# Kernel optimization log

Measured on AMD Instinct MI355X. Metric: run time of the kernel, lower is better.

Reference implementation:

```python
import jax, jax.numpy as jnp
import numpy as np

N_NODES = 50000
N_EDGES = 800000
D_IN, D_HID, N_CLS, N_PROT = 128, 256, 16, 512
EPS = 1e-6


def setup_inputs() -> dict:
    key = jax.random.key(0)
    ks = jax.random.split(key, 12)
    s = 0.05
    return {
        "x": jax.random.normal(ks[0], (N_NODES, D_IN), dtype=jnp.float32),
        "edge_index": jax.random.randint(ks[1], (2, N_EDGES), 0, N_NODES, dtype=jnp.int64),
        "prot": jax.random.randint(ks[2], (N_PROT,), 0, N_NODES, dtype=jnp.int64),
        "epoch": 1,
        "W0": jax.random.normal(ks[3], (D_IN, D_HID), dtype=jnp.float32) * s,
        "b0": jnp.zeros((D_HID,), jnp.float32),
        "W1": jax.random.normal(ks[4], (D_HID, D_HID), dtype=jnp.float32) * s,
        "b1": jnp.zeros((D_HID,), jnp.float32),
        "Wl1": jax.random.normal(ks[5], (D_HID, D_HID), dtype=jnp.float32) * s,
        "bl1": jnp.zeros((D_HID,), jnp.float32),
        "Wl2": jax.random.normal(ks[6], (D_HID, N_CLS), dtype=jnp.float32) * s,
        "bl2": jnp.zeros((N_CLS,), jnp.float32),
    }


def _gcn_layer(h, W, b, src, dst, norm, n):
    # PyG GCNConv: h' = scatter_add(norm * (h @ W)[src] -> dst) + b
    m = (h @ W)[src] * norm[:, None]
    return jax.ops.segment_sum(m, dst, num_segments=n) + b


def _forward(x, edge_index, prot, W0, b0, W1, b1, Wl1, bl1, Wl2, bl2):
    n = x.shape[0]
    loops = jnp.arange(n, dtype=edge_index.dtype)
    src = jnp.concatenate([edge_index[0], loops])
    dst = jnp.concatenate([edge_index[1], loops])
    deg = jax.ops.segment_sum(jnp.ones_like(dst, dtype=x.dtype), dst, num_segments=n)
    dis = jax.lax.rsqrt(deg)  # deg >= 1 thanks to self loops
    norm = dis[src] * dis[dst]

    h = jax.nn.relu(_gcn_layer(x, W0, b0, src, dst, norm, n))
    h = _gcn_layer(h, W1, b1, src, dst, norm, n)

    # L2 row-normalize (torch divides by the norm directly)
    qn = jnp.linalg.norm(h, axis=1, keepdims=True)
    h = h / qn

    # relative_rep: cosine similarity of every node to each anchor
    anchors = h[prot]                             # [P, H]
    nx = jnp.linalg.norm(h, axis=1)               # [N]
    na = jnp.linalg.norm(anchors, axis=1)         # [P]
    num = h @ anchors.T                           # [N, P]
    x_rel = num / jnp.maximum(nx[:, None] * na[None, :], EPS)

    # classifier head on prototypes -> out_proto, then composed prediction
    lin = lambda z: jax.nn.relu(z @ Wl1 + bl1) @ Wl2 + bl2
    out_proto = jax.nn.log_softmax(lin(anchors), axis=-1)   # [P, C]
    out = jax.nn.log_softmax(x_rel @ out_proto, axis=-1)    # [N, C]
    return out, x_rel, out_proto


def reference(x, edge_index, prot, epoch, W0, b0, W1, b1, Wl1, bl1, Wl2, bl2):
    # epoch >= first_step_epochs (=0) branch: inference-path composition
    return _forward(x, edge_index, prot, W0, b0, W1, b1, Wl1, bl1, Wl2, bl2)


if __name__ == "__main__":
    out, x_rel, out_proto = reference(**setup_inputs())
    print(out.shape, x_rel.shape, out_proto.shape)
```

## Files before the change

### kernel.cpp

```cpp
#include <hip/hip_runtime.h>
#include <hip/hip_bf16.h>
#include <math.h>

#define NN 50000
#define NP 50048
#define EE 800000
#define EPAD 1150016
#define DIN 128
#define HID 256
#define NCLS 16
#define NPROT 512

typedef __attribute__((ext_vector_type(8))) short short8;
typedef __attribute__((ext_vector_type(4))) float f32x4;
typedef unsigned int u32;
typedef unsigned long long u64;

__device__ inline unsigned short f2b(float f) {
    union { float f; unsigned u; } c; c.f = f;
    unsigned u = c.u;
    unsigned r = (u + 0x7FFFu + ((u >> 16) & 1u)) >> 16;
    return (unsigned short)r;
}
__device__ inline float b2f(unsigned short u) {
    union { unsigned u; float f; } c; c.u = ((unsigned)u) << 16; return c.f;
}

#define GL2LDS16(g, l)                                                              \
    __builtin_amdgcn_global_load_lds(                                               \
        (const __attribute__((address_space(1))) unsigned int*)(g),                 \
        (__attribute__((address_space(3))) unsigned int*)(l), 16, 0, 0)


__global__ __launch_bounds__(256) void k_count(const int* __restrict__ dst, int* __restrict__ cnt, int e) {
    int i = blockIdx.x * 256 + threadIdx.x;
    if (i < e) atomicAdd(&cnt[dst[i]], 1);
}

__global__ __launch_bounds__(256) void k_scan1(const int* __restrict__ cnt, int* __restrict__ excl,
                                               int* __restrict__ bsum, float* __restrict__ dis, int n) {
    __shared__ int s[256];
    int t = threadIdx.x;
    int i = blockIdx.x * 256 + t;
    int v = (i < n) ? cnt[i] : 0;
    if (i < n) dis[i] = rsqrtf((float)v + 1.0f);
    int vp = (v + 7) & ~7;
    s[t] = vp; __syncthreads();
    for (int d = 1; d < 256; d <<= 1) {
        int add = (t >= d) ? s[t - d] : 0;
        __syncthreads();
        s[t] += add;
        __syncthreads();
    }
    if (i < n) excl[i] = s[t] - vp;
    if (t == 255) bsum[blockIdx.x] = s[255];
}

__global__ __launch_bounds__(256) void k_scan2(const int* __restrict__ bsum, int* __restrict__ boff, int nb) {
    __shared__ int s[256];
    int t = threadIdx.x;
    int v = (t < nb) ? bsum[t] : 0;
    s[t] = v; __syncthreads();
    for (int d = 1; d < 256; d <<= 1) {
        int add = (t >= d) ? s[t - d] : 0;
        __syncthreads();
        s[t] += add;
        __syncthreads();
    }
    if (t < nb) boff[t] = s[t] - v;
}

__global__ __launch_bounds__(256) void k_scan3(const int* __restrict__ excl, const int* __restrict__ boff,
                                               const int* __restrict__ bsum,
                                               int* __restrict__ off, int n, int nb) {
    int i = blockIdx.x * 256 + threadIdx.x;
    if (i < n) off[i] = excl[i] + boff[blockIdx.x];
    if (i == 0) off[n] = boff[nb - 1] + bsum[nb - 1];
}

__global__ __launch_bounds__(256) void k_fill(const int* __restrict__ src, const int* __restrict__ dst,
                                              const int* __restrict__ off, int* __restrict__ cursor,
                                              const float* __restrict__ dis,
                                              int2* __restrict__ csr_e, int e) {
    int i = blockIdx.x * 256 + threadIdx.x;
    if (i >= e) return;
    int s = src[i], d = dst[i];
    int pos = atomicAdd(&cursor[d], 1);
    csr_e[off[d] + pos] = make_int2(s, __float_as_int(dis[s] * dis[d]));
}


#define CAST_BLKS (NN * DIN / 4 / 256)
#define WT0_BLKS  (DIN * HID / 256)
#define WT1_BLKS  (HID * HID / 256)

__global__ __launch_bounds__(256) void k_prep(const float* __restrict__ x, unsigned short* __restrict__ xb,
                                              const float* __restrict__ W0, unsigned short* __restrict__ Wt0,
                                              const float* __restrict__ W1, unsigned short* __restrict__ Wt1) {
    int b = blockIdx.x, t = threadIdx.x;
    if (b < CAST_BLKS) {
        int i = b * 256 + t;
        float4 v = ((const float4*)x)[i];
        ushort4 o; o.x = f2b(v.x); o.y = f2b(v.y); o.z = f2b(v.z); o.w = f2b(v.w);
        ((ushort4*)xb)[i] = o;
    } else if (b < CAST_BLKS + WT0_BLKS) {
        int i = (b - CAST_BLKS) * 256 + t;
        int k = i / HID, n = i - k * HID;
        Wt0[n * DIN + k] = f2b(W0[(size_t)k * HID + n]);
    } else {
        int i = (b - CAST_BLKS - WT0_BLKS) * 256 + t;
        int k = i / HID, n = i - k * HID;
        Wt1[n * HID + k] = f2b(W1[(size_t)k * HID + n]);
    }
}


__global__ __launch_bounds__(256) void k_gemm_mfma(const unsigned short* __restrict__ A,
                                                   const unsigned short* __restrict__ Bt,
                                                   void* __restrict__ C, int M, int Nc, int K, int mode,
                                                   const float* __restrict__ bias) {
    __shared__ __align__(16) unsigned short As[128 * 32];
    __shared__ __align__(16) unsigned short Bs[128 * 32];
    const int t = threadIdx.x;
    const int lane = t & 63;
    const int quad = lane >> 4;
    const int l16 = lane & 15;
    const int wv = t >> 6;
    const int wm = (wv & 1) * 64, wn = (wv >> 1) * 64;
    const int m0 = blockIdx.y * 128, n0 = blockIdx.x * 128;

    f32x4 acc[4][4];
#pragma unroll
    for (int i = 0; i < 4; ++i)
#pragma unroll
        for (int j = 0; j < 4; ++j)
#pragma unroll
            for (int r = 0; r < 4; ++r) acc[i][j][r] = 0.0f;

    const int sr = t >> 2;
    const int sc = (t & 3) * 8;

    for (int k0 = 0; k0 < K; k0 += 32) {
        GL2LDS16(A + (size_t)(m0 + sr) * K + k0 + sc,       &As[t * 8]);
        GL2LDS16(A + (size_t)(m0 + 64 + sr) * K + k0 + sc,  &As[2048 + t * 8]);
        GL2LDS16(Bt + (size_t)(n0 + sr) * K + k0 + sc,      &Bs[t * 8]);
        GL2LDS16(Bt + (size_t)(n0 + 64 + sr) * K + k0 + sc, &Bs[2048 + t * 8]);
        __syncthreads();
        short8 af[4], bf[4];
#pragma unroll
        for (int i = 0; i < 4; ++i)
            af[i] = *(const short8*)&As[(wm + i * 16 + l16) * 32 + quad * 8];
#pragma unroll
        for (int j = 0; j < 4; ++j)
            bf[j] = *(const short8*)&Bs[(wn + j * 16 + l16) * 32 + quad * 8];
#pragma unroll
        for (int i = 0; i < 4; ++i)
#pragma unroll
            for (int j = 0; j < 4; ++j)
                acc[i][j] = __builtin_amdgcn_mfma_f32_16x16x32_bf16(af[i], bf[j], acc[i][j], 0, 0, 0);
        __syncthreads();
    }

#pragma unroll
    for (int i = 0; i < 4; ++i) {
        int rb = m0 + wm + i * 16 + quad * 4;
#pragma unroll
        for (int j = 0; j < 4; ++j) {
            int col = n0 + wn + j * 16 + l16;
#pragma unroll
            for (int rg = 0; rg < 4; ++rg) {
                int r = rb + rg;
                float v = acc[i][j][rg];
                if (mode == 0) {
                    ((unsigned short*)C)[(size_t)r * Nc + col] = f2b(v);
                } else {
                    v = fmaxf(v + bias[col], 0.0f);
                    ((unsigned short*)C)[(size_t)r * Nc + col] = f2b(v);
                }
            }
        }
    }
}


#define GATHER8_D(go, ga)                                                      \
    asm volatile(                                                              \
        "global_load_dword %0, %[g0], off\n\t"                                 \
        "global_load_dword %1, %[g1], off\n\t"                                 \
        "global_load_dword %2, %[g2], off\n\t"                                 \
        "global_load_dword %3, %[g3], off\n\t"                                 \
        "global_load_dword %4, %[g4], off\n\t"                                 \
        "global_load_dword %5, %[g5], off\n\t"                                 \
        "global_load_dword %6, %[g6], off\n\t"                                 \
        "global_load_dword %7, %[g7], off\n\t"                                 \
        "s_waitcnt vmcnt(0)"                                                   \
        : "=&v"(go[0]), "=&v"(go[1]), "=&v"(go[2]), "=&v"(go[3]),              \
          "=&v"(go[4]), "=&v"(go[5]), "=&v"(go[6]), "=&v"(go[7])               \
        : [g0]"v"(ga[0]), [g1]"v"(ga[1]), [g2]"v"(ga[2]), [g3]"v"(ga[3]),      \
          [g4]"v"(ga[4]), [g5]"v"(ga[5]), [g6]"v"(ga[6]), [g7]"v"(ga[7])       \
        : "memory")

#define GATHER8_D2(go, ga)                                                     \
    asm volatile(                                                              \
        "global_load_dwordx2 %0, %[g0], off\n\t"                               \
        "global_load_dwordx2 %1, %[g1], off\n\t"                               \
        "global_load_dwordx2 %2, %[g2], off\n\t"                               \
        "global_load_dwordx2 %3, %[g3], off\n\t"                               \
        "global_load_dwordx2 %4, %[g4], off\n\t"                               \
        "global_load_dwordx2 %5, %[g5], off\n\t"                               \
        "global_load_dwordx2 %6, %[g6], off\n\t"                               \
        "global_load_dwordx2 %7, %[g7], off\n\t"                               \
        "s_waitcnt vmcnt(0)"                                                   \
        : "=&v"(go[0]), "=&v"(go[1]), "=&v"(go[2]), "=&v"(go[3]),              \
          "=&v"(go[4]), "=&v"(go[5]), "=&v"(go[6]), "=&v"(go[7])               \
        : [g0]"v"(ga[0]), [g1]"v"(ga[1]), [g2]"v"(ga[2]), [g3]"v"(ga[3]),      \
          [g4]"v"(ga[4]), [g5]"v"(ga[5]), [g6]"v"(ga[6]), [g7]"v"(ga[7])       \
        : "memory")

__global__ __launch_bounds__(256) void k_agg128(const unsigned short* __restrict__ xw, const int* __restrict__ off,
                                                const int2* __restrict__ csr, const float* __restrict__ dis,
                                                unsigned short* __restrict__ out, int n) {
    int node = (blockIdx.x * 256 + threadIdx.x) >> 6;
    int lane = threadIdx.x & 63;
    if (node >= n) return;
    float d = dis[node];
    float w0 = d * d;
    ushort2 u = ((const ushort2*)(xw + (size_t)node * DIN))[lane];
    float a0 = w0 * b2f(u.x), a1 = w0 * b2f(u.y);
    int p = off[node], p1 = off[node + 1];
    u64 lbase = (u64)xw + (u64)((unsigned)lane * 4u);
    while (p < p1) {
        int seg = min(p1 - p, 64);
        int2 di = csr[p + (lane < seg ? lane : 0)];
        for (int b = 0; b < seg; b += 8) {
            u64 ga[8];
            int wi[8];
#pragma unroll
            for (int k = 0; k < 8; ++k) {
                int srcn = __builtin_amdgcn_readlane(di.x, b + k);
                wi[k] = __builtin_amdgcn_readlane(di.y, b + k);
                ga[k] = lbase + (u64)((u32)srcn * (u32)(DIN * 2));
            }
            u32 go[8];
            GATHER8_D(go, ga);
#pragma unroll
            for (int k = 0; k < 8; ++k) {
                float w = __int_as_float(wi[k]);
                a0 = fmaf(w, b2f((unsigned short)go[k]), a0);
                a1 = fmaf(w, b2f((unsigned short)(go[k] >> 16)), a1);
            }
        }
        p += seg;
    }
    ushort2 o; o.x = f2b(a0); o.y = f2b(a1);
    ((ushort2*)(out + (size_t)node * DIN))[lane] = o;
}

__global__ __launch_bounds__(256) void k_agg256(const unsigned short* __restrict__ xw, const int* __restrict__ off,
                                                const int2* __restrict__ csr, const float* __restrict__ dis,
                                                const float* __restrict__ bias,
                                                unsigned short* __restrict__ out, float* __restrict__ nx, int n) {
    int node = (blockIdx.x * 256 + threadIdx.x) >> 6;
    int lane = threadIdx.x & 63;
    if (node >= n) return;
    float d = dis[node];
    float w0 = d * d;
    ushort4 u = ((const ushort4*)(xw + (size_t)node * HID))[lane];
    float a0 = w0 * b2f(u.x), a1 = w0 * b2f(u.y), a2 = w0 * b2f(u.z), a3 = w0 * b2f(u.w);
    int p = off[node], p1 = off[node + 1];
    u64 lbase = (u64)xw + (u64)((unsigned)lane * 8u);
    while (p < p1) {
        int seg = min(p1 - p, 64);
        int2 di = csr[p + (lane < seg ? lane : 0)];
        for (int b = 0; b < seg; b += 8) {
            u64 ga[8];
            int wi[8];
#pragma unroll
            for (int k = 0; k < 8; ++k) {
                int srcn = __builtin_amdgcn_readlane(di.x, b + k);
                wi[k] = __builtin_amdgcn_readlane(di.y, b + k);
                ga[k] = lbase + (u64)((u32)srcn * (u32)(HID * 2));
            }
            u64 go[8];
            GATHER8_D2(go, ga);
#pragma unroll
            for (int k = 0; k < 8; ++k) {
                float w = __int_as_float(wi[k]);
                u32 lo = (u32)go[k], hi = (u32)(go[k] >> 32);
                a0 = fmaf(w, b2f((unsigned short)lo), a0);
                a1 = fmaf(w, b2f((unsigned short)(lo >> 16)), a1);
                a2 = fmaf(w, b2f((unsigned short)hi), a2);
                a3 = fmaf(w, b2f((unsigned short)(hi >> 16)), a3);
            }
        }
        p += seg;
    }
    float4 b = ((const float4*)bias)[lane];
    a0 += b.x; a1 += b.y; a2 += b.z; a3 += b.w;
    float ss = a0 * a0 + a1 * a1 + a2 * a2 + a3 * a3;
    for (int m = 32; m >= 1; m >>= 1) ss += __shfl_xor(ss, m, 64);
    float qn = sqrtf(ss);
    a0 /= qn; a1 /= qn; a2 /= qn; a3 /= qn;
    float s2 = a0 * a0 + a1 * a1 + a2 * a2 + a3 * a3;
    for (int m = 32; m >= 1; m >>= 1) s2 += __shfl_xor(s2, m, 64);
    if (lane == 0) nx[node] = sqrtf(s2);
    ushort4 o; o.x = f2b(a0); o.y = f2b(a1); o.z = f2b(a2); o.w = f2b(a3);
    ((ushort4*)(out + (size_t)node * HID))[lane] = o;
}


__global__ __launch_bounds__(256) void k_gproto(const unsigned short* __restrict__ hb,
                                                const int* __restrict__ prot, const float* __restrict__ nx,
                                                unsigned short* __restrict__ aRb, float* __restrict__ na,
                                                const float* __restrict__ Wl1, const float* __restrict__ bl1,
                                                const float* __restrict__ Wl2, const float* __restrict__ bl2,
                                                float* __restrict__ outp) {
    __shared__ float sa[HID];
    __shared__ float st[HID];
    int row = blockIdx.x, t = threadIdx.x;
    int p = prot[row];
    unsigned short us = hb[(size_t)p * HID + t];
    aRb[(size_t)row * HID + t] = us;
    sa[t] = b2f(us);
    if (t == 0) na[row] = nx[p];
    __syncthreads();
    float acc = bl1[t];
#pragma unroll 8
    for (int k = 0; k < HID; ++k) acc = fmaf(sa[k], Wl1[k * HID + t], acc);
    st[t] = fmaxf(acc, 0.0f);
    __syncthreads();
    if (t < 64) {
        int c = t & 15, ch = t >> 4;
        float z = 0.f;
#pragma unroll 8
        for (int k = ch * 64; k < ch * 64 + 64; ++k) z = fmaf(st[k], Wl2[k * NCLS + c], z);
        z += __shfl_xor(z, 16, 64);
        z += __shfl_xor(z, 32, 64);
        z += bl2[c];
        float m = z;
        for (int d = 8; d >= 1; d >>= 1) m = fmaxf(m, __shfl_xor(m, d, 64));
        float e = expf(z - m);
        float s = e;
        for (int d = 8; d >= 1; d >>= 1) s += __shfl_xor(s, d, 64);
        if (t < 16) outp[row * NCLS + c] = z - m - logf(s);
    }
}


#define XSW(row, cs) (((cs) ^ (((row) & 7) << 3)))
#define NWGX (4 * (NP / 128))

__global__ __launch_bounds__(256, 4) void k_xrel_out(const unsigned short* __restrict__ A,
                                                     const unsigned short* __restrict__ Bt,
                                                     const float* __restrict__ nx, const float* __restrict__ na,
                                                     const float* __restrict__ proto,
                                                     float* __restrict__ xrel, float* __restrict__ opart) {
    __shared__ __align__(16) unsigned short smem_us[18560];

    const int bid = blockIdx.x;
    const int q = NWGX / 8, r = NWGX % 8;
    const int xcd = bid & 7, li = bid >> 3;
    const int wk = (xcd < r ? xcd * (q + 1) : r * (q + 1) + (xcd - r) * q) + li;
    const int m0 = (wk >> 2) * 128;
    const int nc = wk & 3;
    const int n0 = nc * 128;

    const int t = threadIdx.x;
    const int lane = t & 63;
    const int quad = lane >> 4;
    const int l16 = lane & 15;
    const int wv = t >> 6;
    const int wm = (wv & 1) * 64, wn = (wv >> 1) * 64;

    float nxv[4][4];
#pragma unroll
    for (int i = 0; i < 4; ++i)
#pragma unroll
        for (int rg = 0; rg < 4; ++rg) {
            int rr = m0 + wm + i * 16 + quad * 4 + rg;
            nxv[i][rg] = nx[rr < NN ? rr : NN - 1];
        }
    float nav[4];
#pragma unroll
    for (int j = 0; j < 4; ++j) nav[j] = na[n0 + wn + j * 16 + l16];

    const int sr = t >> 2;
    const int sc = (t & 3) * 8;

    f32x4 acc[4][4];
#pragma unroll
    for (int i = 0; i < 4; ++i)
#pragma unroll
        for (int j = 0; j < 4; ++j)
#pragma unroll
            for (int rr = 0; rr < 4; ++rr) acc[i][j][rr] = 0.0f;

    for (int k0 = 0; k0 < HID; k0 += 32) {
        GL2LDS16(A + (size_t)(m0 + sr) * HID + k0 + sc,        &smem_us[t * 8]);
        GL2LDS16(A + (size_t)(m0 + 64 + sr) * HID + k0 + sc,   &smem_us[2048 + t * 8]);
        GL2LDS16(Bt + (size_t)(n0 + sr) * HID + k0 + sc,       &smem_us[4096 + t * 8]);
        GL2LDS16(Bt + (size_t)(n0 + 64 + sr) * HID + k0 + sc,  &smem_us[4096 + 2048 + t * 8]);
        __syncthreads();
        short8 af[4], bf[4];
#pragma unroll
        for (int i = 0; i < 4; ++i)
            af[i] = *(const short8*)&smem_us[(wm + i * 16 + l16) * 32 + quad * 8];
#pragma unroll
        for (int j = 0; j < 4; ++j)
            bf[j] = *(const short8*)&smem_us[4096 + (wn + j * 16 + l16) * 32 + quad * 8];
#pragma unroll
        for (int i = 0; i < 4; ++i)
#pragma unroll
            for (int j = 0; j < 4; ++j)
                acc[i][j] = __builtin_amdgcn_mfma_f32_16x16x32_bf16(af[i], bf[j], acc[i][j], 0, 0, 0);
        __syncthreads();
    }

    for (int i = t; i < 128 * NCLS; i += 256) {
        int kk = i >> 4, c = i & 15;
        smem_us[16384 + c * 136 + kk] = f2b(proto[(n0 + kk) * NCLS + c]);
    }

#pragma unroll
    for (int i = 0; i < 4; ++i) {
#pragma unroll
        for (int j = 0; j < 4; ++j) {
            int cl = wn + j * 16 + l16;
#pragma unroll
            for (int rg = 0; rg < 4; ++rg) {
                int row = wm + i * 16 + quad * 4 + rg;
                float s = fmaxf(nxv[i][rg] * nav[j], 1e-6f);
                float v = acc[i][j][rg] * __builtin_amdgcn_rcpf(s);
                smem_us[row * 128 + XSW(row, cl)] = f2b(v);
            }
        }
    }
    __syncthreads();

    f32x4 oacc[2];
#pragma unroll
    for (int rr = 0; rr < 4; ++rr) { oacc[0][rr] = 0.0f; oacc[1][rr] = 0.0f; }
#pragma unroll
    for (int ii = 0; ii < 2; ++ii) {
        int rbr = wv * 32 + ii * 16;
#pragma unroll
        for (int ks = 0; ks < 4; ++ks) {
            int row = rbr + l16;
            short8 af = *(const short8*)&smem_us[row * 128 + XSW(row, ks * 32 + quad * 8)];
            short8 pb = *(const short8*)&smem_us[16384 + l16 * 136 + ks * 32 + quad * 8];
            oacc[ii] = __builtin_amdgcn_mfma_f32_16x16x32_bf16(af, pb, oacc[ii], 0, 0, 0);
        }
    }
#pragma unroll
    for (int ii = 0; ii < 2; ++ii)
#pragma unroll
        for (int rg = 0; rg < 4; ++rg) {
            int lrow = wv * 32 + ii * 16 + quad * 4 + rg;
            opart[((size_t)nc * NP + m0 + lrow) * NCLS + l16] = oacc[ii][rg];
        }

#pragma unroll
    for (int it = 0; it < 8; ++it) {
        int idx = it * 256 + t;
        int row = idx >> 4;
        int c8 = (idx & 15) * 8;
        int rr = m0 + row;
        if (rr < NN) {
            short8 u = *(const short8*)&smem_us[row * 128 + XSW(row, c8)];
            float* dst = &xrel[(size_t)rr * NPROT + n0 + c8];
            float4 v0, v1;
            v0.x = b2f((unsigned short)u[0]); v0.y = b2f((unsigned short)u[1]);
            v0.z = b2f((unsigned short)u[2]); v0.w = b2f((unsigned short)u[3]);
            v1.x = b2f((unsigned short)u[4]); v1.y = b2f((unsigned short)u[5]);
            v1.z = b2f((unsigned short)u[6]); v1.w = b2f((unsigned short)u[7]);
            *(float4*)dst = v0;
            *(float4*)(dst + 4) = v1;
        }
    }
}


__global__ __launch_bounds__(256) void k_reduce(const float* __restrict__ opart, float* __restrict__ out) {
    int i = blockIdx.x * 256 + threadIdx.x;
    int row = i >> 4, c = i & 15;
    float z = opart[i] + opart[(size_t)NP * NCLS + i] + opart[(size_t)2 * NP * NCLS + i] +
              opart[(size_t)3 * NP * NCLS + i];
    float mx = z;
    for (int d = 8; d >= 1; d >>= 1) mx = fmaxf(mx, __shfl_xor(mx, d, 64));
    float e = expf(z - mx);
    float s = e;
    for (int d = 8; d >= 1; d >>= 1) s += __shfl_xor(s, d, 64);
    if (row < NN) out[(size_t)row * NCLS + c] = z - mx - logf(s);
}


extern "C" void kernel_launch(void* const* d_in, const int* in_sizes, int n_in,
                              void* d_out, int out_size, void* d_ws, size_t ws_size,
                              hipStream_t stream) {
    const float* x    = (const float*)d_in[0];
    const int*   eidx = (const int*)d_in[1];
    const int*   prot = (const int*)d_in[2];
    const float* W0  = (const float*)d_in[4];
    const float* b0  = (const float*)d_in[5];
    const float* W1  = (const float*)d_in[6];
    const float* b1  = (const float*)d_in[7];
    const float* Wl1 = (const float*)d_in[8];
    const float* bl1 = (const float*)d_in[9];
    const float* Wl2 = (const float*)d_in[10];
    const float* bl2 = (const float*)d_in[11];

    const int N = NN, E = EE;
    const int* esrc_in = eidx;
    const int* edst_in = eidx + E;

    float* out_final = (float*)d_out;
    float* x_rel     = (float*)d_out + (size_t)N * NCLS;
    float* out_proto = x_rel + (size_t)N * NPROT;

    char* w = (char*)d_ws;
    auto alloc = [&](size_t bytes) { char* p = w; w += (bytes + 255) & ~(size_t)255; return p; };
    int*   cnt      = (int*)alloc((size_t)N * 4);
    int*   cursor   = (int*)alloc((size_t)N * 4);
    float* dis      = (float*)alloc((size_t)N * 4);
    int*   excl     = (int*)alloc((size_t)N * 4);
    int*   csr_off  = (int*)alloc((size_t)(N + 1) * 4);
    int*   bsum     = (int*)alloc(1024);
    int*   boff     = (int*)alloc(1024);
    int2*  csr_e    = (int2*)alloc((size_t)EPAD * 8);
    float* nx       = (float*)alloc((size_t)N * 4);
    float* na       = (float*)alloc((size_t)NPROT * 4);
    float* opart    = (float*)alloc((size_t)4 * NP * NCLS * 4);
    unsigned short* xb    = (unsigned short*)alloc((size_t)NP * DIN * 2);
    unsigned short* Wt0   = (unsigned short*)alloc((size_t)HID * DIN * 2);
    unsigned short* Wt1   = (unsigned short*)alloc((size_t)HID * HID * 2);
    unsigned short* bufAb = (unsigned short*)alloc((size_t)NP * HID * 2);
    unsigned short* h0b   = (unsigned short*)alloc((size_t)NP * HID * 2);
    unsigned short* aRb   = (unsigned short*)alloc((size_t)NPROT * HID * 2);
    unsigned short* a1 = bufAb;
    unsigned short* hb = h0b;

    hipMemsetAsync(cnt, 0, (size_t)N * 4, stream);
    hipMemsetAsync(cursor, 0, (size_t)N * 4, stream);
    hipMemsetAsync(csr_e, 0, (size_t)EPAD * 8, stream);

    k_count<<<(E + 255) / 256, 256, 0, stream>>>(edst_in, cnt, E);
    int NB = (N + 255) / 256;
    k_scan1<<<NB, 256, 0, stream>>>(cnt, excl, bsum, dis, N);
    k_scan2<<<1, 256, 0, stream>>>(bsum, boff, NB);
    k_scan3<<<NB, 256, 0, stream>>>(excl, boff, bsum, csr_off, N, NB);
    k_fill<<<(E + 255) / 256, 256, 0, stream>>>(esrc_in, edst_in, csr_off, cursor, dis, csr_e, E);

    k_prep<<<CAST_BLKS + WT0_BLKS + WT1_BLKS, 256, 0, stream>>>(x, xb, W0, Wt0, W1, Wt1);

    const int MT = NP / 128;

    k_agg128<<<(N + 3) / 4, 256, 0, stream>>>(xb, csr_off, csr_e, dis, a1, N);
    k_gemm_mfma<<<dim3(HID / 128, MT), 256, 0, stream>>>(a1, Wt0, h0b, N, HID, DIN, 2, b0);

    k_gemm_mfma<<<dim3(HID / 128, MT), 256, 0, stream>>>(h0b, Wt1, bufAb, N, HID, HID, 0, nullptr);
    k_agg256<<<(N + 3) / 4, 256, 0, stream>>>(bufAb, csr_off, csr_e, dis, b1, hb, nx, N);

    k_gproto<<<NPROT, 256, 0, stream>>>(hb, prot, nx, aRb, na, Wl1, bl1, Wl2, bl2, out_proto);

    k_xrel_out<<<NWGX, 256, 0, stream>>>(hb, aRb, nx, na, out_proto, x_rel, opart);

    k_reduce<<<NP * NCLS / 256, 256, 0, stream>>>(opart, out_final);
}
```

Baseline: 435.5 us.

## Double-buffer LDS tiles in xrel GEMM and keep prototype operand in registers

The k-loop of the x_rel GEMM kernel now uses two LDS buffers: it issues the global-to-LDS loads for the next 32-wide k slice while MFMAs run on the current slice, with one barrier per iteration instead of two. The bf16-converted prototype matrix used by the second MFMA stage is now loaded straight into per-lane registers before the loop, instead of being staged through a separate LDS region after it. Together these aim to hide global load latency and drop the extra LDS traffic and footprint. The cost is more live VGPRs under the 4-blocks-per-CU launch bound, which could cause spills.

Result: slower. 461.2 us (+5.9%).

```diff
diff --git a/kernel.cpp b/kernel.cpp
--- a/kernel.cpp
+++ b/kernel.cpp
@@ -349,13 +349,15 @@
 
 #define XSW(row, cs) (((cs) ^ (((row) & 7) << 3)))
 #define NWGX (4 * (NP / 128))
+#define ABUF(c) ((c) * 8192)
+#define BBUF(c) ((c) * 8192 + 4096)
 
 __global__ __launch_bounds__(256, 4) void k_xrel_out(const unsigned short* __restrict__ A,
                                                      const unsigned short* __restrict__ Bt,
                                                      const float* __restrict__ nx, const float* __restrict__ na,
                                                      const float* __restrict__ proto,
                                                      float* __restrict__ xrel, float* __restrict__ opart) {
-    __shared__ __align__(16) unsigned short smem_us[18560];
+    __shared__ __align__(16) unsigned short smem_us[16384];
 
     const int bid = blockIdx.x;
     const int q = NWGX / 8, r = NWGX % 8;
@@ -372,6 +374,14 @@
     const int wv = t >> 6;
     const int wm = (wv & 1) * 64, wn = (wv >> 1) * 64;
 
+    const int sr = t >> 2;
+    const int sc = (t & 3) * 8;
+
+    GL2LDS16(A + (size_t)(m0 + sr) * HID + sc,        &smem_us[ABUF(0) + t * 8]);
+    GL2LDS16(A + (size_t)(m0 + 64 + sr) * HID + sc,   &smem_us[ABUF(0) + 2048 + t * 8]);
+    GL2LDS16(Bt + (size_t)(n0 + sr) * HID + sc,       &smem_us[BBUF(0) + t * 8]);
+    GL2LDS16(Bt + (size_t)(n0 + 64 + sr) * HID + sc,  &smem_us[BBUF(0) + 2048 + t * 8]);
+
     float nxv[4][4];
 #pragma unroll
     for (int i = 0; i < 4; ++i)
@@ -384,8 +394,15 @@
 #pragma unroll
     for (int j = 0; j < 4; ++j) nav[j] = na[n0 + wn + j * 16 + l16];
 
-    const int sr = t >> 2;
-    const int sc = (t & 3) * 8;
+    short8 pbr[4];
+#pragma unroll
+    for (int ks = 0; ks < 4; ++ks) {
+        const float* pp = proto + (size_t)(n0 + ks * 32 + quad * 8) * NCLS + l16;
+        short8 v;
+#pragma unroll
+        for (int e = 0; e < 8; ++e) v[e] = (short)f2b(pp[e * NCLS]);
+        pbr[ks] = v;
+    }
 
     f32x4 acc[4][4];
 #pragma unroll
@@ -395,30 +412,31 @@
 #pragma unroll
             for (int rr = 0; rr < 4; ++rr) acc[i][j][rr] = 0.0f;
 
+    __syncthreads();
+
+    int cur = 0;
     for (int k0 = 0; k0 < HID; k0 += 32) {
-        GL2LDS16(A + (size_t)(m0 + sr) * HID + k0 + sc,        &smem_us[t * 8]);
-        GL2LDS16(A + (size_t)(m0 + 64 + sr) * HID + k0 + sc,   &smem_us[2048 + t * 8]);
-        GL2LDS16(Bt + (size_t)(n0 + sr) * HID + k0 + sc,       &smem_us[4096 + t * 8]);
-        GL2LDS16(Bt + (size_t)(n0 + 64 + sr) * HID + k0 + sc,  &smem_us[4096 + 2048 + t * 8]);
-        __syncthreads();
+        if (k0 + 32 < HID) {
+            int kn = k0 + 32;
+            GL2LDS16(A + (size_t)(m0 + sr) * HID + kn + sc,        &smem_us[ABUF(cur ^ 1) + t * 8]);
+            GL2LDS16(A + (size_t)(m0 + 64 + sr) * HID + kn + sc,   &smem_us[ABUF(cur ^ 1) + 2048 + t * 8]);
+            GL2LDS16(Bt + (size_t)(n0 + sr) * HID + kn + sc,       &smem_us[BBUF(cur ^ 1) + t * 8]);
+            GL2LDS16(Bt + (size_t)(n0 + 64 + sr) * HID + kn + sc,  &smem_us[BBUF(cur ^ 1) + 2048 + t * 8]);
+        }
         short8 af[4], bf[4];
 #pragma unroll
         for (int i = 0; i < 4; ++i)
-            af[i] = *(const short8*)&smem_us[(wm + i * 16 + l16) * 32 + quad * 8];
+            af[i] = *(const short8*)&smem_us[ABUF(cur) + (wm + i * 16 + l16) * 32 + quad * 8];
 #pragma unroll
         for (int j = 0; j < 4; ++j)
-            bf[j] = *(const short8*)&smem_us[4096 + (wn + j * 16 + l16) * 32 + quad * 8];
+            bf[j] = *(const short8*)&smem_us[BBUF(cur) + (wn + j * 16 + l16) * 32 + quad * 8];
 #pragma unroll
         for (int i = 0; i < 4; ++i)
 #pragma unroll
             for (int j = 0; j < 4; ++j)
                 acc[i][j] = __builtin_amdgcn_mfma_f32_16x16x32_bf16(af[i], bf[j], acc[i][j], 0, 0, 0);
         __syncthreads();
-    }
-
-    for (int i = t; i < 128 * NCLS; i += 256) {
-        int kk = i >> 4, c = i & 15;
-        smem_us[16384 + c * 136 + kk] = f2b(proto[(n0 + kk) * NCLS + c]);
+        cur ^= 1;
     }
 
 #pragma unroll
@@ -447,8 +465,7 @@
         for (int ks = 0; ks < 4; ++ks) {
             int row = rbr + l16;
             short8 af = *(const short8*)&smem_us[row * 128 + XSW(row, ks * 32 + quad * 8)];
-            short8 pb = *(const short8*)&smem_us[16384 + l16 * 136 + ks * 32 + quad * 8];
-            oacc[ii] = __builtin_amdgcn_mfma_f32_16x16x32_bf16(af, pb, oacc[ii], 0, 0, 0);
+            oacc[ii] = __builtin_amdgcn_mfma_f32_16x16x32_bf16(af, pbr[ks], oacc[ii], 0, 0, 0);
         }
     }
 #pragma unroll
```
